# Performance work log

Hardware: AMD Instinct MI355X
Metric: run time of the kernel (lower is better)

The kernel has to match this reference:

```python
import jax, jax.numpy as jnp
import numpy as np

D_MODEL = 1024
D_FF = 4096
NUM_EXPERTS = 8
TOP_K = 2


def setup_inputs() -> dict:
    key = jax.random.key(0)
    ks = jax.random.split(key, 10)
    s = 0.02
    x = jax.random.normal(ks[0], (2, 1024, D_MODEL), dtype=jnp.float32)
    # router gate (nn.Linear(d_model, num_experts))
    Wr = jax.random.normal(ks[1], (D_MODEL, NUM_EXPERTS), dtype=jnp.float32) * s
    br = jnp.zeros((NUM_EXPERTS,), dtype=jnp.float32)
    # stacked expert weights
    Wg = jax.random.normal(ks[2], (NUM_EXPERTS, D_MODEL, D_FF), dtype=jnp.float32) * s
    bg = jnp.zeros((NUM_EXPERTS, D_FF), dtype=jnp.float32)
    Wu = jax.random.normal(ks[3], (NUM_EXPERTS, D_MODEL, D_FF), dtype=jnp.float32) * s
    bu = jnp.zeros((NUM_EXPERTS, D_FF), dtype=jnp.float32)
    Wd = jax.random.normal(ks[4], (NUM_EXPERTS, D_FF, D_MODEL), dtype=jnp.float32) * s
    bd = jnp.zeros((NUM_EXPERTS, D_MODEL), dtype=jnp.float32)
    return {"x": x, "Wr": Wr, "br": br, "Wg": Wg, "bg": bg,
            "Wu": Wu, "bu": bu, "Wd": Wd, "bd": bd}


def reference(x, Wr, br, Wg, bg, Wu, bu, Wd, bd):
    B, S, D = x.shape
    E = Wg.shape[0]
    xt = x.reshape(-1, D)                       # [T, d]
    T = xt.shape[0]
    # router: softmax in float32, top-k, renormalize (Mixtral-style)
    logits = xt @ Wr + br                       # [T, E]
    probs = jax.nn.softmax(logits.astype(jnp.float32), axis=-1)
    rw, sel = jax.lax.top_k(probs, TOP_K)       # [T, K]
    rw = rw / jnp.sum(rw, axis=-1, keepdims=True)
    # per-token per-expert combine weight (0 if expert not selected)
    w_full = jnp.zeros((T, E), dtype=rw.dtype).at[
        jnp.arange(T)[:, None], sel].add(rw)    # [T, E]
    # SwiGLU experts, computed densely over all tokens then masked-combined
    g = jnp.einsum('td,edf->etf', xt, Wg) + bg[:, None, :]   # [E, T, f]
    u = jnp.einsum('td,edf->etf', xt, Wu) + bu[:, None, :]
    h = jax.nn.silu(g) * u
    y = jnp.einsum('etf,efd->etd', h, Wd) + bd[:, None, :]    # [E, T, d]
    out = jnp.einsum('te,etd->td', w_full.astype(x.dtype), y)
    return out.reshape(B, S, D)
```

## Files before the change

kernel.cpp:

```cpp
#include <hip/hip_runtime.h>

typedef float floatx4 __attribute__((ext_vector_type(4)));
typedef __bf16 bf16x4 __attribute__((ext_vector_type(4)));
typedef __bf16 bf16x8 __attribute__((ext_vector_type(8)));

#define D_MODEL 1024
#define D_FF 4096
#define NE 8

__device__ __forceinline__ void gload16(const void* g, void* l) {
    __builtin_amdgcn_global_load_lds(
        (const __attribute__((address_space(1))) void*)g,
        (__attribute__((address_space(3))) void*)l, 16, 0, 0);
}

__device__ __forceinline__ int frag_off(int row, int q) {
    return row * 32 + ((q ^ ((row >> 2) & 3)) << 3);
}

__global__ __launch_bounds__(256) void router_kernel(
    const float* __restrict__ x, const float* __restrict__ Wr,
    const float* __restrict__ br, int* __restrict__ cnt,
    int* __restrict__ list, float* __restrict__ w_slot, int T)
{
    int wv = threadIdx.x >> 6;
    int lane = threadIdx.x & 63;
    int t = blockIdx.x * 4 + wv;
    if (t >= T) return;

    const float* xp = x + (size_t)t * D_MODEL;
    float acc[8] = {0.f,0.f,0.f,0.f,0.f,0.f,0.f,0.f};
#pragma unroll
    for (int i = 0; i < 16; ++i) {
        int d = i * 64 + lane;
        float xv = xp[d];
        float4 w0 = *(const float4*)(Wr + d * 8);
        float4 w1 = *(const float4*)(Wr + d * 8 + 4);
        acc[0] += xv * w0.x; acc[1] += xv * w0.y;
        acc[2] += xv * w0.z; acc[3] += xv * w0.w;
        acc[4] += xv * w1.x; acc[5] += xv * w1.y;
        acc[6] += xv * w1.z; acc[7] += xv * w1.w;
    }
#pragma unroll
    for (int off = 32; off >= 1; off >>= 1) {
#pragma unroll
        for (int e = 0; e < 8; ++e)
            acc[e] += __shfl_down(acc[e], off, 64);
    }
    if (lane == 0) {
        float l[8];
#pragma unroll
        for (int e = 0; e < 8; ++e) l[e] = acc[e] + br[e];
        int i0 = 0; float v0 = l[0];
#pragma unroll
        for (int e = 1; e < 8; ++e) if (l[e] > v0) { v0 = l[e]; i0 = e; }
        int i1 = -1; float v1 = -3.4e38f;
#pragma unroll
        for (int e = 0; e < 8; ++e) if (e != i0 && l[e] > v1) { v1 = l[e]; i1 = e; }
        float ex = __expf(v1 - v0);
        float w0 = 1.f / (1.f + ex);
        float w1 = ex / (1.f + ex);
        int p0 = atomicAdd(&cnt[i0], 1);
        list[i0 * T + p0] = 2 * t;
        int p1 = atomicAdd(&cnt[i1], 1);
        list[i1 * T + p1] = 2 * t + 1;
        w_slot[2 * t]     = w0;
        w_slot[2 * t + 1] = w1;
    }
}

__global__ __launch_bounds__(256) void prep_kernel(
    const float* __restrict__ Wg, const float* __restrict__ Wu,
    const float* __restrict__ Wd, const float* __restrict__ x,
    __bf16* __restrict__ Wgt, __bf16* __restrict__ Wut,
    __bf16* __restrict__ Wdt, __bf16* __restrict__ Xb)
{
    const int bid = blockIdx.x;
    const int tid = threadIdx.x;
    if (bid >= 24576) {
        int base = (bid - 24576) * 2048 + tid * 8;
        float4 v0 = *(const float4*)(x + base);
        float4 v1 = *(const float4*)(x + base + 4);
        bf16x8 o = {(__bf16)v0.x, (__bf16)v0.y, (__bf16)v0.z, (__bf16)v0.w,
                    (__bf16)v1.x, (__bf16)v1.y, (__bf16)v1.z, (__bf16)v1.w};
        *(bf16x8*)(Xb + base) = o;
        return;
    }
    const int tensor = bid >> 13;
    const int rem = bid & 8191;
    const int e = rem >> 10;
    const int tile = rem & 1023;
    const float* src; __bf16* dst; int K, N, kb, nb;
    if (tensor == 0)      { src = Wg; dst = Wgt; }
    else if (tensor == 1) { src = Wu; dst = Wut; }
    else                  { src = Wd; dst = Wdt; }
    if (tensor < 2) { K = 1024; N = 4096; kb = (tile & 15) << 6; nb = (tile >> 4) << 6; }
    else            { K = 4096; N = 1024; kb = (tile & 63) << 6; nb = (tile >> 6) << 6; }
    src += (size_t)e * K * N;
    dst += (size_t)e * K * N;

    __shared__ __bf16 tileT[64 * 72];
    const int kr = (tid >> 4) << 2;
    const int nc = (tid & 15) << 2;
    const float* s0 = src + (size_t)(kb + kr) * N + nb + nc;
    float4 r0 = *(const float4*)(s0);
    float4 r1 = *(const float4*)(s0 + N);
    float4 r2 = *(const float4*)(s0 + 2 * N);
    float4 r3 = *(const float4*)(s0 + 3 * N);
    bf16x4 c0 = {(__bf16)r0.x, (__bf16)r1.x, (__bf16)r2.x, (__bf16)r3.x};
    bf16x4 c1 = {(__bf16)r0.y, (__bf16)r1.y, (__bf16)r2.y, (__bf16)r3.y};
    bf16x4 c2 = {(__bf16)r0.z, (__bf16)r1.z, (__bf16)r2.z, (__bf16)r3.z};
    bf16x4 c3 = {(__bf16)r0.w, (__bf16)r1.w, (__bf16)r2.w, (__bf16)r3.w};
    *(bf16x4*)&tileT[(nc + 0) * 72 + kr] = c0;
    *(bf16x4*)&tileT[(nc + 1) * 72 + kr] = c1;
    *(bf16x4*)&tileT[(nc + 2) * 72 + kr] = c2;
    *(bf16x4*)&tileT[(nc + 3) * 72 + kr] = c3;
    __syncthreads();
#pragma unroll
    for (int i = 0; i < 2; ++i) {
        int p = i * 256 + tid;
        int n = p >> 3, kg = p & 7;
        bf16x8 v = *(const bf16x8*)&tileT[n * 72 + kg * 8];
        *(bf16x8*)(dst + (size_t)(nb + n) * K + kb + kg * 8) = v;
    }
}

__global__ __launch_bounds__(256, 3) void gateup3_kernel(
    const __bf16* __restrict__ Xb, const __bf16* __restrict__ Wgt,
    const __bf16* __restrict__ Wut, const float* __restrict__ bg,
    const float* __restrict__ bu, const int* __restrict__ cnt,
    const int* __restrict__ list, __bf16* __restrict__ H, int T)
{
    const int e  = blockIdx.z;
    const int m0 = blockIdx.y * 128;
    const int n0 = blockIdx.x * 64;
    const int count = cnt[e];
    if (m0 >= count) return;

    __shared__ __bf16 ldsA[4096];
    __shared__ __bf16 ldsBg[2048];
    __shared__ __bf16 ldsBu[2048];
    __shared__ int s_entry[128];

    const int tid = threadIdx.x;
    if (tid < 128) {
        int r = m0 + tid;
        s_entry[tid] = (r < count) ? list[e * T + r] : list[e * T];
    }
    __syncthreads();

    const int row0 = tid >> 2, j0 = tid & 3;
    const int g0 = j0 ^ ((row0 >> 2) & 3);
    const int p1 = 256 + tid, row1 = p1 >> 2, j1 = p1 & 3;
    const int g1 = j1 ^ ((row1 >> 2) & 3);
    const __bf16* asrc0 = Xb + (size_t)(s_entry[row0] >> 1) * D_MODEL + g0 * 8;
    const __bf16* asrc1 = Xb + (size_t)(s_entry[row1] >> 1) * D_MODEL + g1 * 8;
    const __bf16* gsrc  = Wgt + ((size_t)e * D_FF + n0 + row0) * D_MODEL + g0 * 8;
    const __bf16* usrc  = Wut + ((size_t)e * D_FF + n0 + row0) * D_MODEL + g0 * 8;
    char* adst0 = (char*)ldsA + tid * 16;
    char* adst1 = (char*)ldsA + (256 + tid) * 16;
    char* gdst  = (char*)ldsBg + tid * 16;
    char* udst  = (char*)ldsBu + tid * 16;

    const int wv = tid >> 6, lane = tid & 63;
    const int wm = wv >> 1, wn = wv & 1;
    const int q = lane >> 4, ln = lane & 15;
    int aoff[4], boff[2];
#pragma unroll
    for (int i = 0; i < 4; ++i) aoff[i] = frag_off(wm * 64 + i * 16 + ln, q);
#pragma unroll
    for (int i = 0; i < 2; ++i) boff[i] = frag_off(wn * 32 + i * 16 + ln, q);

    floatx4 accg[4][2] = {};
    floatx4 accu[4][2] = {};

    for (int k0 = 0; k0 < D_MODEL; k0 += 32) {
        gload16(asrc0 + k0, adst0);
        gload16(asrc1 + k0, adst1);
        gload16(gsrc + k0, gdst);
        gload16(usrc + k0, udst);
        __syncthreads();

        bf16x8 af[4], bgf[2], buf[2];
#pragma unroll
        for (int i = 0; i < 4; ++i) af[i]  = *(const bf16x8*)&ldsA[aoff[i]];
#pragma unroll
        for (int i = 0; i < 2; ++i) bgf[i] = *(const bf16x8*)&ldsBg[boff[i]];
#pragma unroll
        for (int i = 0; i < 2; ++i) buf[i] = *(const bf16x8*)&ldsBu[boff[i]];
#pragma unroll
        for (int mi = 0; mi < 4; ++mi)
#pragma unroll
            for (int ni = 0; ni < 2; ++ni) {
                accg[mi][ni] = __builtin_amdgcn_mfma_f32_16x16x32_bf16(af[mi], bgf[ni], accg[mi][ni], 0, 0, 0);
                accu[mi][ni] = __builtin_amdgcn_mfma_f32_16x16x32_bf16(af[mi], buf[ni], accu[mi][ni], 0, 0, 0);
            }
        __syncthreads();
    }

#pragma unroll
    for (int ni = 0; ni < 2; ++ni) {
        int col = n0 + wn * 32 + ni * 16 + ln;
        float bgv = bg[e * D_FF + col];
        float buv = bu[e * D_FF + col];
#pragma unroll
        for (int mi = 0; mi < 4; ++mi) {
            int lrow0 = wm * 64 + mi * 16 + q * 4;
#pragma unroll
            for (int r = 0; r < 4; ++r) {
                int lr = lrow0 + r;
                if (m0 + lr < count) {
                    int entry = s_entry[lr];
                    float g = accg[mi][ni][r] + bgv;
                    float u = accu[mi][ni][r] + buv;
                    float h = g / (1.f + __expf(-g)) * u;
                    H[(size_t)entry * D_FF + col] = (__bf16)h;
                }
            }
        }
    }
}

__global__ __launch_bounds__(256, 3) void down3_kernel(
    const __bf16* __restrict__ H, const __bf16* __restrict__ Wdt,
    const float* __restrict__ bd, const int* __restrict__ cnt,
    const int* __restrict__ list, float* __restrict__ Y, int T)
{
    const int e  = blockIdx.z >> 2;
    const int kc = blockIdx.z & 3;
    const int m0 = blockIdx.y * 128;
    const int n0 = blockIdx.x * 128;
    const int count = cnt[e];
    if (m0 >= count) return;

    __shared__ __bf16 ldsA[4096];
    __shared__ __bf16 ldsB[4096];
    __shared__ int s_entry[128];

    const int tid = threadIdx.x;
    if (tid < 128) {
        int r = m0 + tid;
        s_entry[tid] = (r < count) ? list[e * T + r] : list[e * T];
    }
    __syncthreads();

    const int kbase = kc * (D_FF / 4);
    const __bf16* asrc[2]; const __bf16* bsrc[2];
    char* adst[2]; char* bdst[2];
#pragma unroll
    for (int i = 0; i < 2; ++i) {
        int p = i * 256 + tid;
        int row = p >> 2, j = p & 3;
        int g = j ^ ((row >> 2) & 3);
        asrc[i] = H + (size_t)s_entry[row] * D_FF + kbase + g * 8;
        bsrc[i] = Wdt + ((size_t)e * D_MODEL + n0 + row) * D_FF + kbase + g * 8;
        adst[i] = (char*)ldsA + (size_t)p * 16;
        bdst[i] = (char*)ldsB + (size_t)p * 16;
    }

    const int wv = tid >> 6, lane = tid & 63;
    const int wm = wv >> 1, wn = wv & 1;
    const int q = lane >> 4, ln = lane & 15;
    int aoff[4], boff[4];
#pragma unroll
    for (int i = 0; i < 4; ++i) {
        aoff[i] = frag_off(wm * 64 + i * 16 + ln, q);
        boff[i] = frag_off(wn * 64 + i * 16 + ln, q);
    }

    floatx4 acc[4][4] = {};

    for (int k0 = 0; k0 < D_FF / 4; k0 += 32) {
#pragma unroll
        for (int i = 0; i < 2; ++i) {
            gload16(asrc[i] + k0, adst[i]);
            gload16(bsrc[i] + k0, bdst[i]);
        }
        __syncthreads();

        bf16x8 af[4], bf[4];
#pragma unroll
        for (int i = 0; i < 4; ++i) af[i] = *(const bf16x8*)&ldsA[aoff[i]];
#pragma unroll
        for (int i = 0; i < 4; ++i) bf[i] = *(const bf16x8*)&ldsB[boff[i]];
#pragma unroll
        for (int mi = 0; mi < 4; ++mi)
#pragma unroll
            for (int ni = 0; ni < 4; ++ni)
                acc[mi][ni] = __builtin_amdgcn_mfma_f32_16x16x32_bf16(af[mi], bf[ni], acc[mi][ni], 0, 0, 0);
        __syncthreads();
    }

    const size_t kc_off = (size_t)kc * 2 * T * D_MODEL;
#pragma unroll
    for (int ni = 0; ni < 4; ++ni) {
        int col = n0 + wn * 64 + ni * 16 + ln;
        float bdv = (kc == 0) ? bd[e * D_MODEL + col] : 0.f;
#pragma unroll
        for (int mi = 0; mi < 4; ++mi) {
            int lrow0 = wm * 64 + mi * 16 + q * 4;
#pragma unroll
            for (int r = 0; r < 4; ++r) {
                int lr = lrow0 + r;
                if (m0 + lr < count) {
                    int entry = s_entry[lr];
                    Y[kc_off + (size_t)entry * D_MODEL + col] = acc[mi][ni][r] + bdv;
                }
            }
        }
    }
}

__global__ __launch_bounds__(256) void combine_kernel(
    const float* __restrict__ Y, const float* __restrict__ w_slot,
    float* __restrict__ out, int T)
{
    int idx = blockIdx.x * 256 + threadIdx.x;
    int t = idx >> 8;
    const float4* Y4 = (const float4*)Y;
    size_t r0 = (size_t)(2 * t) * 256 + (idx & 255);
    size_t r1 = r0 + 256;
    size_t ks = (size_t)2 * T * 256;
    float4 a = Y4[r0], b = Y4[r1];
#pragma unroll
    for (int kc = 1; kc < 4; ++kc) {
        float4 va = Y4[r0 + kc * ks], vb = Y4[r1 + kc * ks];
        a.x += va.x; a.y += va.y; a.z += va.z; a.w += va.w;
        b.x += vb.x; b.y += vb.y; b.z += vb.z; b.w += vb.w;
    }
    float w0 = w_slot[2 * t], w1 = w_slot[2 * t + 1];
    float4 o = {w0 * a.x + w1 * b.x, w0 * a.y + w1 * b.y,
                w0 * a.z + w1 * b.z, w0 * a.w + w1 * b.w};
    ((float4*)out)[idx] = o;
}

extern "C" void kernel_launch(void* const* d_in, const int* in_sizes, int n_in,
                              void* d_out, int out_size, void* d_ws, size_t ws_size,
                              hipStream_t stream) {
    const float* x  = (const float*)d_in[0];
    const float* Wr = (const float*)d_in[1];
    const float* br = (const float*)d_in[2];
    const float* Wg = (const float*)d_in[3];
    const float* bg = (const float*)d_in[4];
    const float* Wu = (const float*)d_in[5];
    const float* bu = (const float*)d_in[6];
    const float* Wd = (const float*)d_in[7];
    const float* bd = (const float*)d_in[8];
    float* out = (float*)d_out;
    const int T = in_sizes[0] / D_MODEL;

    char* ws = (char*)d_ws;
    size_t off = 256;
    int*   cnt    = (int*)ws;
    int*   list   = (int*)(ws + off);              off += (size_t)NE * T * 4;
    float* w_slot = (float*)(ws + off);            off += (size_t)2 * T * 4;
    off = (off + 1023) & ~(size_t)1023;
    __bf16* Xb  = (__bf16*)(ws + off);             off += (size_t)T * D_MODEL * 2;
    __bf16* H   = (__bf16*)(ws + off);             off += (size_t)2 * T * D_FF * 2;
    __bf16* Wgt = (__bf16*)(ws + off);
    float*  Y   = (float*)(ws + off);
    off += (size_t)NE * D_MODEL * D_FF * 2;
    __bf16* Wut = (__bf16*)(ws + off);             off += (size_t)NE * D_MODEL * D_FF * 2;
    __bf16* Wdt = (__bf16*)(ws + off);             off += (size_t)NE * D_FF * D_MODEL * 2;

    hipMemsetAsync(cnt, 0, 256, stream);

    router_kernel<<<dim3((T + 3) / 4), dim3(256), 0, stream>>>(x, Wr, br, cnt, list, w_slot, T);

    prep_kernel<<<dim3(25600), dim3(256), 0, stream>>>(Wg, Wu, Wd, x, Wgt, Wut, Wdt, Xb);

    dim3 gb(D_FF / 64, (T + 127) / 128, NE);
    gateup3_kernel<<<gb, dim3(256), 0, stream>>>(Xb, Wgt, Wut, bg, bu, cnt, list, H, T);

    dim3 gc(D_MODEL / 128, (T + 127) / 128, NE * 4);
    down3_kernel<<<gc, dim3(256), 0, stream>>>(H, Wdt, bd, cnt, list, Y, T);

    combine_kernel<<<dim3(T * D_MODEL / 4 / 256), dim3(256), 0, stream>>>(Y, w_slot, out, T);
}
```

Measured before the change: 677.8 us.

## Rewrite weight transpose with packed bf16 pairs and halve down-proj split-K

The weight prep transpose now has each thread read two rows, pack matching elements into 32-bit bf16 pairs, and store them in a padded uint LDS tile. Each thread then writes 32 contiguous bytes per output row, which should cut LDS bank conflicts and improve store width. Separately, the down-projection split-K factor drops from 4 to 2. That halves the partial Y buffers the combine kernel must read and sum, at the cost of fewer blocks and longer K loops per block.

```diff
diff --git a/kernel.cpp b/kernel.cpp
--- a/kernel.cpp
+++ b/kernel.cpp
@@ -1,6 +1,7 @@
 #include <hip/hip_runtime.h>
 
 typedef float floatx4 __attribute__((ext_vector_type(4)));
+typedef __bf16 bf16x2 __attribute__((ext_vector_type(2)));
 typedef __bf16 bf16x4 __attribute__((ext_vector_type(4)));
 typedef __bf16 bf16x8 __attribute__((ext_vector_type(8)));
 
@@ -16,6 +17,12 @@
 
 __device__ __forceinline__ int frag_off(int row, int q) {
     return row * 32 + ((q ^ ((row >> 2) & 3)) << 3);
+}
+
+__device__ __forceinline__ unsigned int pk(float lo, float hi) {
+    union { bf16x2 v; unsigned int u; } c;
+    c.v = bf16x2{(__bf16)lo, (__bf16)hi};
+    return c.u;
 }
 
 __global__ __launch_bounds__(256) void router_kernel(
@@ -96,33 +103,39 @@
     else                  { src = Wd; dst = Wdt; }
     if (tensor < 2) { K = 1024; N = 4096; kb = (tile & 15) << 6; nb = (tile >> 4) << 6; }
     else            { K = 4096; N = 1024; kb = (tile & 63) << 6; nb = (tile >> 6) << 6; }
-    src += (size_t)e * K * N;
-    dst += (size_t)e * K * N;
-
-    __shared__ __bf16 tileT[64 * 72];
-    const int kr = (tid >> 4) << 2;
-    const int nc = (tid & 15) << 2;
-    const float* s0 = src + (size_t)(kb + kr) * N + nb + nc;
-    float4 r0 = *(const float4*)(s0);
-    float4 r1 = *(const float4*)(s0 + N);
-    float4 r2 = *(const float4*)(s0 + 2 * N);
-    float4 r3 = *(const float4*)(s0 + 3 * N);
-    bf16x4 c0 = {(__bf16)r0.x, (__bf16)r1.x, (__bf16)r2.x, (__bf16)r3.x};
-    bf16x4 c1 = {(__bf16)r0.y, (__bf16)r1.y, (__bf16)r2.y, (__bf16)r3.y};
-    bf16x4 c2 = {(__bf16)r0.z, (__bf16)r1.z, (__bf16)r2.z, (__bf16)r3.z};
-    bf16x4 c3 = {(__bf16)r0.w, (__bf16)r1.w, (__bf16)r2.w, (__bf16)r3.w};
-    *(bf16x4*)&tileT[(nc + 0) * 72 + kr] = c0;
-    *(bf16x4*)&tileT[(nc + 1) * 72 + kr] = c1;
-    *(bf16x4*)&tileT[(nc + 2) * 72 + kr] = c2;
-    *(bf16x4*)&tileT[(nc + 3) * 72 + kr] = c3;
+    src += (size_t)e * K * N + (size_t)kb * N + nb;
+    dst += (size_t)e * K * N + (size_t)nb * K + kb;
+
+    __shared__ unsigned int tp[64 * 33];
+
+    const int p  = tid >> 3;
+    const int ci = tid & 7;
+    const float* s0 = src + (size_t)(2 * p) * N + 4 * ci;
+    float4 r0a = *(const float4*)(s0);
+    float4 r0b = *(const float4*)(s0 + 32);
+    float4 r1a = *(const float4*)(s0 + N);
+    float4 r1b = *(const float4*)(s0 + N + 32);
+
+    unsigned int* w0 = &tp[(4 * ci) * 33 + p];
+    w0[0]  = pk(r0a.x, r1a.x);
+    w0[33] = pk(r0a.y, r1a.y);
+    w0[66] = pk(r0a.z, r1a.z);
+    w0[99] = pk(r0a.w, r1a.w);
+    unsigned int* w1 = &tp[(4 * ci + 32) * 33 + p];
+    w1[0]  = pk(r0b.x, r1b.x);
+    w1[33] = pk(r0b.y, r1b.y);
+    w1[66] = pk(r0b.z, r1b.z);
+    w1[99] = pk(r0b.w, r1b.w);
     __syncthreads();
-#pragma unroll
-    for (int i = 0; i < 2; ++i) {
-        int p = i * 256 + tid;
-        int n = p >> 3, kg = p & 7;
-        bf16x8 v = *(const bf16x8*)&tileT[n * 72 + kg * 8];
-        *(bf16x8*)(dst + (size_t)(nb + n) * K + kb + kg * 8) = v;
-    }
+
+    const int r = tid >> 2;
+    const int q = tid & 3;
+    const unsigned int* rp = &tp[r * 33 + q * 8];
+    uint4 oa = {rp[0], rp[1], rp[2], rp[3]};
+    uint4 ob = {rp[4], rp[5], rp[6], rp[7]};
+    __bf16* drow = dst + (size_t)r * K + q * 16;
+    *(uint4*)(drow)     = oa;
+    *(uint4*)(drow + 8) = ob;
 }
 
 __global__ __launch_bounds__(256, 3) void gateup3_kernel(
@@ -226,8 +239,8 @@
     const float* __restrict__ bd, const int* __restrict__ cnt,
     const int* __restrict__ list, float* __restrict__ Y, int T)
 {
-    const int e  = blockIdx.z >> 2;
-    const int kc = blockIdx.z & 3;
+    const int e  = blockIdx.z >> 1;
+    const int kc = blockIdx.z & 1;
     const int m0 = blockIdx.y * 128;
     const int n0 = blockIdx.x * 128;
     const int count = cnt[e];
@@ -244,7 +257,7 @@
     }
     __syncthreads();
 
-    const int kbase = kc * (D_FF / 4);
+    const int kbase = kc * (D_FF / 2);
     const __bf16* asrc[2]; const __bf16* bsrc[2];
     char* adst[2]; char* bdst[2];
 #pragma unroll
@@ -270,7 +283,7 @@
 
     floatx4 acc[4][4] = {};
 
-    for (int k0 = 0; k0 < D_FF / 4; k0 += 32) {
+    for (int k0 = 0; k0 < D_FF / 2; k0 += 32) {
 #pragma unroll
         for (int i = 0; i < 2; ++i) {
             gload16(asrc[i] + k0, adst[i]);
@@ -323,7 +336,7 @@
     size_t ks = (size_t)2 * T * 256;
     float4 a = Y4[r0], b = Y4[r1];
 #pragma unroll
-    for (int kc = 1; kc < 4; ++kc) {
+    for (int kc = 1; kc < 2; ++kc) {
         float4 va = Y4[r0 + kc * ks], vb = Y4[r1 + kc * ks];
         a.x += va.x; a.y += va.y; a.z += va.z; a.w += va.w;
         b.x += vb.x; b.y += vb.y; b.z += vb.z; b.w += vb.w;
@@ -372,7 +385,7 @@
     dim3 gb(D_FF / 64, (T + 127) / 128, NE);
     gateup3_kernel<<<gb, dim3(256), 0, stream>>>(Xb, Wgt, Wut, bg, bu, cnt, list, H, T);
 
-    dim3 gc(D_MODEL / 128, (T + 127) / 128, NE * 4);
+    dim3 gc(D_MODEL / 128, (T + 127) / 128, NE * 2);
     down3_kernel<<<gc, dim3(256), 0, stream>>>(H, Wdt, bd, cnt, list, Y, T);
 
     combine_kernel<<<dim3(T * D_MODEL / 4 / 256), dim3(256), 0, stream>>>(Y, w_slot, out, T);
```

Result: no change. 675.0 us (-0.4%).
